# Kernel optimization log

Hardware: AMD Instinct MI355X
Metric: run time of the kernel (lower is better)

## Reference

```python
import jax, jax.numpy as jnp
import numpy as np

NUM_EMBEDDINGS = 1024
EMBEDDING_DIM = 64
COMMITMENT_COST = 0.25
DECAY = 0.99
EPSILON = 1e-05
N_TOKENS = 131072


def setup_inputs() -> dict:
    key = jax.random.key(0)
    k1, k2, k3 = jax.random.split(key, 3)
    inputs = jax.random.normal(k1, (N_TOKENS, EMBEDDING_DIM), dtype=jnp.float32)
    embed_w = jax.random.normal(k2, (NUM_EMBEDDINGS, EMBEDDING_DIM), dtype=jnp.float32)
    ema_w = jax.random.normal(k3, (NUM_EMBEDDINGS, EMBEDDING_DIM), dtype=jnp.float32)
    ema_cluster_size = jnp.zeros((NUM_EMBEDDINGS,), dtype=jnp.float32)
    return {"inputs": inputs, "embed_w": embed_w, "ema_w": ema_w,
            "ema_cluster_size": ema_cluster_size}


def reference(inputs, embed_w, ema_w, ema_cluster_size):
    K = embed_w.shape[0]
    # squared L2 distances [N, K]
    distances = (jnp.sum(inputs ** 2, axis=1, keepdims=True)
                 + jnp.sum(embed_w ** 2, axis=1)
                 - 2.0 * inputs @ embed_w.T)
    encoding_indices = jnp.argmin(distances, axis=1)          # [N]
    encodings = jax.nn.one_hot(encoding_indices, K, dtype=inputs.dtype)  # [N, K]

    # EMA updates (training branch in the torch module)
    cluster_size = ema_cluster_size * DECAY + (1.0 - DECAY) * jnp.sum(encodings, axis=0)
    n = jnp.sum(cluster_size)
    cluster_size = (cluster_size + EPSILON) / (n + K * EPSILON) * n  # Laplace smoothing
    dw = jax.ops.segment_sum(inputs, encoding_indices, num_segments=K)  # == encodings.T @ inputs
    ema_w_new = ema_w * DECAY + (1.0 - DECAY) * dw
    embedding_new = ema_w_new / cluster_size[:, None]

    quantized = embedding_new[encoding_indices]               # == encodings @ embedding_new
    e_latent_loss = jnp.mean(0.5 * jnp.sum((jax.lax.stop_gradient(quantized) - inputs) ** 2, axis=1))
    loss = COMMITMENT_COST * e_latent_loss
    quantized = inputs + jax.lax.stop_gradient(quantized - inputs)  # straight-through

    avg_probs = jnp.mean(encodings, axis=0)
    perplexity = jnp.exp(-jnp.sum(avg_probs * jnp.log(avg_probs + 1e-10)))
    return (loss, quantized, perplexity, encodings)
```

## Files before the change

### kernel.cpp

```cpp
#include <hip/hip_runtime.h>
#include <hip/hip_fp16.h>

#define N_TOK 131072
#define KCODES 1024
#define DIM 64
#define QUANT_OFF 1
#define PERP_OFF 8388609
#define ENC_OFF ((size_t)8388610)
#define EPS_SUSPECT 4e-3f

typedef __attribute__((ext_vector_type(8))) unsigned short ushort8v;
typedef __attribute__((ext_vector_type(8))) _Float16 half8v;
typedef __attribute__((ext_vector_type(4))) float f32x4;

__device__ __forceinline__ float wave_reduce_sum(float v) {
    #pragma unroll
    for (int o = 32; o > 0; o >>= 1) v += __shfl_xor(v, o, 64);
    return v;
}

__device__ __forceinline__ void cvt8h(const float4 a, const float4 b,
                                      half8v* h, half8v* l) {
    float f[8] = {a.x, a.y, a.z, a.w, b.x, b.y, b.z, b.w};
    #pragma unroll
    for (int j = 0; j < 8; ++j) {
        _Float16 hh = (_Float16)f[j];
        float fh = (float)hh;
        _Float16 ll = (_Float16)(f[j] - fh);
        (*h)[j] = hh;
        (*l)[j] = ll;
    }
}

__global__ void k0_prep(const float* __restrict__ ew, float* __restrict__ cbuf,
                        unsigned short* __restrict__ ewh, unsigned short* __restrict__ ewl,
                        float* __restrict__ dwacc, unsigned* __restrict__ suspcnt) {
    int tid = threadIdx.x;
    int lane = tid & 63;
    int wg = blockIdx.x * 4 + (tid >> 6);
    int gt = blockIdx.x * 256 + tid;
    if (gt == 0) *suspcnt = 0u;
    #pragma unroll
    for (int z = 0; z < 8; ++z) {
        int e = gt * 8 + z;
        float v = ew[e];
        _Float16 hh = (_Float16)v;
        float fh = (float)hh;
        _Float16 ll = (_Float16)(v - fh);
        unsigned short uh, ul;
        __builtin_memcpy(&uh, &hh, 2);
        __builtin_memcpy(&ul, &ll, 2);
        ewh[e] = uh;
        ewl[e] = ul;
        dwacc[e] = 0.0f;
    }
    #pragma unroll
    for (int k = 0; k < 8; ++k) {
        int row = wg * 8 + k;
        float v = ew[row * 64 + lane];
        float s = wave_reduce_sum(v * v);
        if (lane == 0) cbuf[row] = 0.5f * s;
    }
}

__global__ __launch_bounds__(256) void k1_argmin(
        const float* __restrict__ x, const unsigned short* __restrict__ ewh,
        const unsigned short* __restrict__ ewl, const float* __restrict__ cbuf,
        float* __restrict__ out, unsigned* __restrict__ idxbuf,
        unsigned* __restrict__ susp, unsigned* __restrict__ suspcnt) {
    __shared__ unsigned short EH[128 * 64];
    __shared__ unsigned short EL[128 * 64];
    __shared__ float scc[128];

    int tid = threadIdx.x;
    int lane = tid & 63;
    int wv = tid >> 6;
    int l15 = lane & 15;
    int l4 = lane >> 4;
    size_t t0 = (size_t)blockIdx.x * 128;
    size_t t0w = t0 + (size_t)wv * 32;

    half8v ah[2][2], al[2][2];
    #pragma unroll
    for (int rt = 0; rt < 2; ++rt) {
        const float* xp = x + (t0w + rt * 16 + l15) * 64 + l4 * 8;
        #pragma unroll
        for (int s = 0; s < 2; ++s) {
            float4 a = *(const float4*)(xp + s * 32);
            float4 b = *(const float4*)(xp + s * 32 + 4);
            cvt8h(a, b, &ah[rt][s], &al[rt][s]);
        }
    }

    float m1[2][4], m2[2][4];
    int i1[2][4], i2[2][4];
    #pragma unroll
    for (int rt = 0; rt < 2; ++rt)
        #pragma unroll
        for (int r = 0; r < 4; ++r) {
            m1[rt][r] = -3.4e38f; m2[rt][r] = -3.4e38f;
            i1[rt][r] = 0; i2[rt][r] = 0;
        }

    for (int ch = 0; ch < 8; ++ch) {
        int c0 = ch * 128;
        {
            int r = tid >> 1, h = tid & 1;
            const unsigned short* gh = ewh + (size_t)(c0 + r) * 64 + h * 32;
            const unsigned short* gl = ewl + (size_t)(c0 + r) * 64 + h * 32;
            #pragma unroll
            for (int q = 0; q < 4; ++q) {
                ushort8v hv = *(const ushort8v*)(gh + q * 8);
                ushort8v lv = *(const ushort8v*)(gl + q * 8);
                int byteoff = (r * 128 + h * 64 + q * 16) ^ ((r & 7) << 4);
                *(ushort8v*)((char*)EH + byteoff) = hv;
                *(ushort8v*)((char*)EL + byteoff) = lv;
            }
            if (tid < 128) scc[tid] = cbuf[c0 + tid];
        }
        __syncthreads();

        {
            float* base = out + ENC_OFF + (t0 + (size_t)ch * 16) * 1024;
            float4 z4; z4.x = z4.y = z4.z = z4.w = 0.0f;
            float2 z2; z2.x = z2.y = 0.0f;
            float4* b4 = (float4*)(base + 2);
            #pragma unroll 4
            for (int u = 0; u < 16; ++u) {
                int slot = u * 256 + tid;
                if (slot < 4095) b4[slot] = z4;
            }
            if (tid == 0) *(float2*)base = z2;
            if (tid == 255) *(float2*)(base + 16382) = z2;
        }

        #pragma unroll 2
        for (int ct = 0; ct < 8; ++ct) {
            int crow = ct * 16 + l15;
            int swz = (crow & 7) << 4;
            int b0 = (crow * 128 + l4 * 16) ^ swz;
            int b1 = (crow * 128 + 64 + l4 * 16) ^ swz;
            half8v bh0 = *(half8v*)((char*)EH + b0);
            half8v bl0 = *(half8v*)((char*)EL + b0);
            half8v bh1 = *(half8v*)((char*)EH + b1);
            half8v bl1 = *(half8v*)((char*)EL + b1);
            float sccv = scc[crow];
            int cid = c0 + crow;
            #pragma unroll
            for (int rt = 0; rt < 2; ++rt) {
                f32x4 acc = {0.f, 0.f, 0.f, 0.f};
                acc = __builtin_amdgcn_mfma_f32_16x16x32_f16(ah[rt][0], bh0, acc, 0, 0, 0);
                acc = __builtin_amdgcn_mfma_f32_16x16x32_f16(al[rt][0], bh0, acc, 0, 0, 0);
                acc = __builtin_amdgcn_mfma_f32_16x16x32_f16(ah[rt][0], bl0, acc, 0, 0, 0);
                acc = __builtin_amdgcn_mfma_f32_16x16x32_f16(ah[rt][1], bh1, acc, 0, 0, 0);
                acc = __builtin_amdgcn_mfma_f32_16x16x32_f16(al[rt][1], bh1, acc, 0, 0, 0);
                acc = __builtin_amdgcn_mfma_f32_16x16x32_f16(ah[rt][1], bl1, acc, 0, 0, 0);
                #pragma unroll
                for (int r = 0; r < 4; ++r) {
                    float sc = acc[r] - sccv;
                    if (sc > m1[rt][r]) {
                        m2[rt][r] = m1[rt][r]; i2[rt][r] = i1[rt][r];
                        m1[rt][r] = sc; i1[rt][r] = cid;
                    } else if (sc > m2[rt][r]) {
                        m2[rt][r] = sc; i2[rt][r] = cid;
                    }
                }
            }
        }
        __syncthreads();
    }

    #pragma unroll
    for (int rt = 0; rt < 2; ++rt)
        #pragma unroll
        for (int r = 0; r < 4; ++r) {
            float m1v = m1[rt][r], m2v = m2[rt][r];
            int i1v = i1[rt][r], i2v = i2[rt][r];
            #pragma unroll
            for (int o = 1; o < 16; o <<= 1) {
                float b1 = __shfl_xor(m1v, o, 64); int bi1 = __shfl_xor(i1v, o, 64);
                float b2 = __shfl_xor(m2v, o, 64); int bi2 = __shfl_xor(i2v, o, 64);
                if (b1 > m1v || (b1 == m1v && bi1 < i1v)) {
                    float c2v; int c2i;
                    if (m1v > b2 || (m1v == b2 && i1v < bi2)) { c2v = m1v; c2i = i1v; }
                    else { c2v = b2; c2i = bi2; }
                    m1v = b1; i1v = bi1; m2v = c2v; i2v = c2i;
                } else {
                    if (b1 > m2v || (b1 == m2v && bi1 < i2v)) { m2v = b1; i2v = bi1; }
                }
            }
            if (l15 == 0) {
                size_t tok = t0w + rt * 16 + l4 * 4 + r;
                idxbuf[tok] = (unsigned)i1v;
                if (m2v >= m1v - EPS_SUSPECT) {
                    unsigned p = atomicAdd(suspcnt, 1u);
                    susp[p] = (unsigned)tok;
                }
            }
        }
}

__global__ void k1s_resolve(const float* __restrict__ x, const float* __restrict__ ew,
                            const float* __restrict__ cbuf, const unsigned* __restrict__ susp,
                            const unsigned* __restrict__ suspcnt, unsigned* __restrict__ idxbuf) {
    int lane = threadIdx.x & 63;
    int wid = blockIdx.x * 4 + (threadIdx.x >> 6);
    unsigned n = *suspcnt;
    for (unsigned s = wid; s < n; s += 256) {
        unsigned tok = susp[s];
        float4 xr[16];
        const float4* xp = (const float4*)(x + (size_t)tok * 64);
        #pragma unroll
        for (int q = 0; q < 16; ++q) xr[q] = xp[q];
        float best = -3.4e38f;
        int bidx = 0;
        for (int rr = 0; rr < 16; ++rr) {
            int code = rr * 64 + lane;
            const float4* ep = (const float4*)(ew + (size_t)code * 64);
            float d = 0.0f;
            #pragma unroll
            for (int q = 0; q < 16; ++q) {
                float4 xv = xr[q];
                float4 e = ep[q];
                d = fmaf(xv.x, e.x, d); d = fmaf(xv.y, e.y, d);
                d = fmaf(xv.z, e.z, d); d = fmaf(xv.w, e.w, d);
            }
            float sc = d - cbuf[code];
            if (sc > best) { best = sc; bidx = code; }
        }
        #pragma unroll
        for (int o = 1; o < 64; o <<= 1) {
            float vo = __shfl_xor(best, o, 64);
            int io = __shfl_xor(bidx, o, 64);
            if (vo > best || (vo == best && io < bidx)) { best = vo; bidx = io; }
        }
        if (lane == 0) idxbuf[tok] = (unsigned)bidx;
    }
}

__global__ void k1h_hist(unsigned* __restrict__ idxbuf, unsigned* __restrict__ blockhist) {
    __shared__ unsigned hist[1024];
    int tid = threadIdx.x;
    #pragma unroll
    for (int q = 0; q < 4; ++q) hist[q * 256 + tid] = 0u;
    __syncthreads();
    if (tid < 128) {
        size_t tok = (size_t)blockIdx.x * 128 + tid;
        unsigned bin = idxbuf[tok];
        unsigned rank = atomicAdd(&hist[bin], 1u);
        idxbuf[tok] = bin | (rank << 10);
    }
    __syncthreads();
    #pragma unroll
    for (int q = 0; q < 4; ++q)
        blockhist[(size_t)blockIdx.x * 1024 + q * 256 + tid] = hist[q * 256 + tid];
}

__global__ void k2a_scan(const unsigned* __restrict__ blockhist,
                         unsigned* __restrict__ blockbase,
                         unsigned* __restrict__ counts) {
    int lane = threadIdx.x & 63;
    int bin = blockIdx.x * 4 + (threadIdx.x >> 6);
    unsigned v[16];
    unsigned s = 0;
    #pragma unroll
    for (int j = 0; j < 16; ++j) v[j] = blockhist[(size_t)(lane * 16 + j) * 1024 + bin];
    #pragma unroll
    for (int j = 0; j < 16; ++j) { unsigned t = v[j]; v[j] = s; s += t; }
    unsigned inc = s;
    for (int o = 1; o < 64; o <<= 1) {
        unsigned n = __shfl_up(inc, o, 64);
        if (lane >= o) inc += n;
    }
    unsigned excl = inc - s;
    #pragma unroll
    for (int j = 0; j < 16; ++j)
        blockbase[(size_t)(lane * 16 + j) * 1024 + bin] = excl + v[j];
    if (lane == 63) counts[bin] = inc;
}

__global__ void k2_stats(const float* __restrict__ ema_cs, const unsigned* __restrict__ counts,
                         float* __restrict__ smoothed, unsigned* __restrict__ offsets,
                         float* __restrict__ out) {
    __shared__ float sfw[16];
    __shared__ unsigned scw[16];
    __shared__ float nsh;
    int t = threadIdx.x;
    int lane = t & 63, w = t >> 6;
    unsigned cnt = counts[t];
    float cs = 0.99f * ema_cs[t] + 0.01f * (float)cnt;

    float s = wave_reduce_sum(cs);
    if (lane == 0) sfw[w] = s;
    __syncthreads();
    if (t == 0) {
        float n = 0.f;
        #pragma unroll
        for (int j = 0; j < 16; ++j) n += sfw[j];
        nsh = n;
    }
    __syncthreads();
    float n = nsh;
    smoothed[t] = (cs + 1e-5f) / (n + 1024.0f * 1e-5f) * n;

    unsigned inc = cnt;
    #pragma unroll
    for (int o = 1; o < 64; o <<= 1) {
        unsigned v = __shfl_up(inc, o, 64);
        if (lane >= o) inc += v;
    }
    if (lane == 63) scw[w] = inc;
    __syncthreads();
    unsigned wb = 0;
    #pragma unroll
    for (int j = 0; j < 16; ++j) if (j < w) wb += scw[j];
    offsets[t] = wb + inc - cnt;

    float p = (float)cnt / 131072.0f;
    float term = p * logf(p + 1e-10f);
    float ps = wave_reduce_sum(term);
    if (lane == 0) sfw[w] = ps;
    __syncthreads();
    if (t == 0) {
        float e = 0.f;
        #pragma unroll
        for (int j = 0; j < 16; ++j) e += sfw[j];
        out[PERP_OFF] = expf(-e);
    }
}

__global__ void k3_scatter(const unsigned* __restrict__ idxbuf,
                           const unsigned* __restrict__ offsets,
                           const unsigned* __restrict__ blockbase,
                           int* __restrict__ toklist, int* __restrict__ clustid,
                           float* __restrict__ out) {
    int i = blockIdx.x * 256 + threadIdx.x;
    unsigned v = idxbuf[i];
    unsigned bin = v & 1023u;
    unsigned rank = v >> 10;
    unsigned pos = offsets[bin] + blockbase[(size_t)(i >> 7) * 1024 + bin] + rank;
    toklist[pos] = i;
    clustid[pos] = (int)bin;
    out[ENC_OFF + (size_t)i * 1024 + bin] = 1.0f;
}

__global__ void k4a_dw(const float* __restrict__ x, const int* __restrict__ toklist,
                       const int* __restrict__ clustid, float* __restrict__ dwacc) {
    int lane = threadIdx.x & 63, w = threadIdx.x >> 6;
    int p0 = blockIdx.x * 128 + w * 32;
    int cur = clustid[p0];
    float acc = 0.0f;
    #pragma unroll 4
    for (int t = 0; t < 32; ++t) {
        int pos = p0 + t;
        int c = clustid[pos];
        int tok = toklist[pos];
        float v = x[(size_t)tok * 64 + lane];
        if (c != cur) {
            atomicAdd(&dwacc[(size_t)cur * 64 + lane], acc);
            acc = 0.0f; cur = c;
        }
        acc += v;
    }
    atomicAdd(&dwacc[(size_t)cur * 64 + lane], acc);
}

__global__ void k4b_emb(const float* __restrict__ emaw, const float* __restrict__ dwacc,
                        const float* __restrict__ smoothed, float* __restrict__ embnew) {
    int t = blockIdx.x * 256 + threadIdx.x;
    int k = t >> 6;
    embnew[t] = (emaw[t] * 0.99f + 0.01f * dwacc[t]) / smoothed[k];
}

__global__ void k5_output(const float* __restrict__ x, const float* __restrict__ embnew,
                          const unsigned* __restrict__ idxbuf, float* __restrict__ out,
                          float* __restrict__ partials) {
    __shared__ float red[4];
    int tid = threadIdx.x;
    int gid = blockIdx.x * 256 + tid;
    size_t i = (size_t)(gid >> 4);
    int c = (gid & 15) * 4;
    unsigned ii = idxbuf[i] & 1023u;
    float4 xv = *(const float4*)(x + i * 64 + c);
    float4 q = *(const float4*)(embnew + (size_t)ii * 64 + c);
    float* o = out + QUANT_OFF + i * 64 + c;
    float d0 = q.x - xv.x, d1 = q.y - xv.y, d2 = q.z - xv.z, d3 = q.w - xv.w;
    o[0] = xv.x + d0; o[1] = xv.y + d1; o[2] = xv.z + d2; o[3] = xv.w + d3;
    float ls = d0 * d0 + d1 * d1 + d2 * d2 + d3 * d3;
    ls = wave_reduce_sum(ls);
    if ((tid & 63) == 0) red[tid >> 6] = ls;
    __syncthreads();
    if (tid == 0) partials[blockIdx.x] = red[0] + red[1] + red[2] + red[3];
}

__global__ void k6_loss(const float* __restrict__ partials, float* __restrict__ out) {
    __shared__ float red[4];
    int tid = threadIdx.x;
    float s = 0.0f;
    #pragma unroll 8
    for (int j = 0; j < 32; ++j) s += partials[tid + j * 256];
    s = wave_reduce_sum(s);
    if ((tid & 63) == 0) red[tid >> 6] = s;
    __syncthreads();
    if (tid == 0) out[0] = 0.125f * (red[0] + red[1] + red[2] + red[3]) / 131072.0f;
}

extern "C" void kernel_launch(void* const* d_in, const int* in_sizes, int n_in,
                              void* d_out, int out_size, void* d_ws, size_t ws_size,
                              hipStream_t stream) {
    const float* x     = (const float*)d_in[0];
    const float* ew    = (const float*)d_in[1];
    const float* emaw  = (const float*)d_in[2];
    const float* emacs = (const float*)d_in[3];
    float* out = (float*)d_out;
    float* wsf = (float*)d_ws;

    float*          cbuf      = wsf;
    float*          smoothed  = wsf + 1024;
    unsigned*       offsets   = (unsigned*)(wsf + 2048);
    unsigned*       counts    = (unsigned*)(wsf + 3072);
    float*          partials  = wsf + 4096;
    unsigned*       suspcnt   = (unsigned*)(wsf + 12288);
    unsigned*       idxbuf    = (unsigned*)(wsf + 12352);
    unsigned*       susp      = idxbuf + N_TOK;
    int*            toklist   = (int*)(susp + N_TOK);
    int*            clustid   = toklist + N_TOK;
    float*          dwacc     = wsf + 12352 + 4 * N_TOK;
    float*          embnew    = dwacc + 65536;
    unsigned*       blockhist = (unsigned*)(embnew + 65536);
    unsigned*       blockbase = blockhist + 1024 * 1024;
    unsigned short* ewh       = (unsigned short*)(blockbase + 1024 * 1024);
    unsigned short* ewl       = ewh + 65536;

    hipLaunchKernelGGL(k0_prep,    dim3(32),   dim3(256),  0, stream, ew, cbuf, ewh, ewl, dwacc, suspcnt);
    hipLaunchKernelGGL(k1_argmin,  dim3(1024), dim3(256),  0, stream, x, ewh, ewl, cbuf, out, idxbuf, susp, suspcnt);
    hipLaunchKernelGGL(k1s_resolve,dim3(64),   dim3(256),  0, stream, x, ew, cbuf, susp, suspcnt, idxbuf);
    hipLaunchKernelGGL(k1h_hist,   dim3(1024), dim3(256),  0, stream, idxbuf, blockhist);
    hipLaunchKernelGGL(k2a_scan,   dim3(256),  dim3(256),  0, stream, blockhist, blockbase, counts);
    hipLaunchKernelGGL(k2_stats,   dim3(1),    dim3(1024), 0, stream, emacs, counts, smoothed, offsets, out);
    hipLaunchKernelGGL(k3_scatter, dim3(512),  dim3(256),  0, stream, idxbuf, offsets, blockbase, toklist, clustid, out);
    hipLaunchKernelGGL(k4a_dw,     dim3(1024), dim3(256),  0, stream, x, toklist, clustid, dwacc);
    hipLaunchKernelGGL(k4b_emb,    dim3(256),  dim3(256),  0, stream, emaw, dwacc, smoothed, embnew);
    hipLaunchKernelGGL(k5_output,  dim3(8192), dim3(256),  0, stream, x, embnew, idxbuf, out, partials);
    hipLaunchKernelGGL(k6_loss,    dim3(1),    dim3(256),  0, stream, partials, out);
}
```

Baseline: 731.5 us.

## Move one-hot encoding writes out of argmin into a dedicated kernel

The zero-fill of the 512 MB one-hot output is removed from the argmin kernel, along with the scattered 1.0 writes in the scatter kernel. A new kernel writes each full one-hot row directly from the final indices after suspect resolution. This drops the read-modify-write of scattered ones and lets argmin run as pure compute. The cost is that the big store no longer overlaps with the MFMA argmin work.

```diff
diff --git a/kernel.cpp b/kernel.cpp
--- a/kernel.cpp
+++ b/kernel.cpp
@@ -66,8 +66,8 @@
 __global__ __launch_bounds__(256) void k1_argmin(
         const float* __restrict__ x, const unsigned short* __restrict__ ewh,
         const unsigned short* __restrict__ ewl, const float* __restrict__ cbuf,
-        float* __restrict__ out, unsigned* __restrict__ idxbuf,
-        unsigned* __restrict__ susp, unsigned* __restrict__ suspcnt) {
+        unsigned* __restrict__ idxbuf, unsigned* __restrict__ susp,
+        unsigned* __restrict__ suspcnt) {
     __shared__ unsigned short EH[128 * 64];
     __shared__ unsigned short EL[128 * 64];
     __shared__ float scc[128];
@@ -119,20 +119,6 @@
             if (tid < 128) scc[tid] = cbuf[c0 + tid];
         }
         __syncthreads();
-
-        {
-            float* base = out + ENC_OFF + (t0 + (size_t)ch * 16) * 1024;
-            float4 z4; z4.x = z4.y = z4.z = z4.w = 0.0f;
-            float2 z2; z2.x = z2.y = 0.0f;
-            float4* b4 = (float4*)(base + 2);
-            #pragma unroll 4
-            for (int u = 0; u < 16; ++u) {
-                int slot = u * 256 + tid;
-                if (slot < 4095) b4[slot] = z4;
-            }
-            if (tid == 0) *(float2*)base = z2;
-            if (tid == 255) *(float2*)(base + 16382) = z2;
-        }
 
         #pragma unroll 2
         for (int ct = 0; ct < 8; ++ct) {
@@ -238,6 +224,37 @@
     }
 }
 
+__global__ __launch_bounds__(256) void k_enc(const unsigned* __restrict__ idxbuf,
+                                             float* __restrict__ out) {
+    __shared__ unsigned sidx[64];
+    int tid = threadIdx.x;
+    size_t t0 = (size_t)blockIdx.x * 64;
+    if (tid < 64) sidx[tid] = idxbuf[t0 + tid] & 1023u;
+    __syncthreads();
+    #pragma unroll 2
+    for (int u = 0; u < 64; ++u) {
+        int idx = (int)sidx[u];
+        float* base = out + ENC_OFF + (t0 + u) * 1024;
+        if (tid < 255) {
+            int f0 = 2 + tid * 4;
+            float4 v;
+            v.x = (f0 + 0 == idx) ? 1.0f : 0.0f;
+            v.y = (f0 + 1 == idx) ? 1.0f : 0.0f;
+            v.z = (f0 + 2 == idx) ? 1.0f : 0.0f;
+            v.w = (f0 + 3 == idx) ? 1.0f : 0.0f;
+            ((float4*)(base + 2))[tid] = v;
+        } else {
+            float2 h, tl;
+            h.x = (idx == 0) ? 1.0f : 0.0f;
+            h.y = (idx == 1) ? 1.0f : 0.0f;
+            tl.x = (idx == 1022) ? 1.0f : 0.0f;
+            tl.y = (idx == 1023) ? 1.0f : 0.0f;
+            *(float2*)base = h;
+            *(float2*)(base + 1022) = tl;
+        }
+    }
+}
+
 __global__ void k1h_hist(unsigned* __restrict__ idxbuf, unsigned* __restrict__ blockhist) {
     __shared__ unsigned hist[1024];
     int tid = threadIdx.x;
@@ -332,8 +349,7 @@
 __global__ void k3_scatter(const unsigned* __restrict__ idxbuf,
                            const unsigned* __restrict__ offsets,
                            const unsigned* __restrict__ blockbase,
-                           int* __restrict__ toklist, int* __restrict__ clustid,
-                           float* __restrict__ out) {
+                           int* __restrict__ toklist, int* __restrict__ clustid) {
     int i = blockIdx.x * 256 + threadIdx.x;
     unsigned v = idxbuf[i];
     unsigned bin = v & 1023u;
@@ -341,7 +357,6 @@
     unsigned pos = offsets[bin] + blockbase[(size_t)(i >> 7) * 1024 + bin] + rank;
     toklist[pos] = i;
     clustid[pos] = (int)bin;
-    out[ENC_OFF + (size_t)i * 1024 + bin] = 1.0f;
 }
 
 __global__ void k4a_dw(const float* __restrict__ x, const int* __restrict__ toklist,
@@ -433,12 +448,13 @@
     unsigned short* ewl       = ewh + 65536;
 
     hipLaunchKernelGGL(k0_prep,    dim3(32),   dim3(256),  0, stream, ew, cbuf, ewh, ewl, dwacc, suspcnt);
-    hipLaunchKernelGGL(k1_argmin,  dim3(1024), dim3(256),  0, stream, x, ewh, ewl, cbuf, out, idxbuf, susp, suspcnt);
+    hipLaunchKernelGGL(k1_argmin,  dim3(1024), dim3(256),  0, stream, x, ewh, ewl, cbuf, idxbuf, susp, suspcnt);
     hipLaunchKernelGGL(k1s_resolve,dim3(64),   dim3(256),  0, stream, x, ew, cbuf, susp, suspcnt, idxbuf);
+    hipLaunchKernelGGL(k_enc,      dim3(2048), dim3(256),  0, stream, idxbuf, out);
     hipLaunchKernelGGL(k1h_hist,   dim3(1024), dim3(256),  0, stream, idxbuf, blockhist);
     hipLaunchKernelGGL(k2a_scan,   dim3(256),  dim3(256),  0, stream, blockhist, blockbase, counts);
     hipLaunchKernelGGL(k2_stats,   dim3(1),    dim3(1024), 0, stream, emacs, counts, smoothed, offsets, out);
-    hipLaunchKernelGGL(k3_scatter, dim3(512),  dim3(256),  0, stream, idxbuf, offsets, blockbase, toklist, clustid, out);
+    hipLaunchKernelGGL(k3_scatter, dim3(512),  dim3(256),  0, stream, idxbuf, offsets, blockbase, toklist, clustid);
     hipLaunchKernelGGL(k4a_dw,     dim3(1024), dim3(256),  0, stream, x, toklist, clustid, dwacc);
     hipLaunchKernelGGL(k4b_emb,    dim3(256),  dim3(256),  0, stream, emaw, dwacc, smoothed, embnew);
     hipLaunchKernelGGL(k5_output,  dim3(8192), dim3(256),  0, stream, x, embnew, idxbuf, out, partials);
```

After: 820.8 us. +12.2%, slower.
